# Optimization experiments

Measured on AMD Instinct MI355X. Metric: run time of the kernel, lower is better.

## Reference

```python
import jax, jax.numpy as jnp
import numpy as np

B, L, DIM, H = 2, 2048, 2048, 16
DH = DIM // H  # 128, size_per_head


def setup_inputs() -> dict:
    key = jax.random.key(0)
    k1, k2, k3, k4, k5, k6 = jax.random.split(key, 6)
    s = 0.02
    return {
        "query_tensor": jax.random.normal(k1, (B, L, DIM), jnp.float32),
        "value_tensor": jax.random.normal(k2, (B, L, DIM), jnp.float32),
        "attention_mask": jax.random.randint(k3, (B, L), 0, 2).astype(jnp.float32),
        "Wq": jax.random.normal(k4, (DIM, DIM), jnp.float32) * s,
        "Wk": jax.random.normal(k5, (DIM, DIM), jnp.float32) * s,
        "Wv": jax.random.normal(k6, (DIM, DIM), jnp.float32) * s,
    }


def reference(query_tensor, value_tensor, attention_mask, Wq, Wk, Wv):
    b, lq, dim = query_tensor.shape
    lv = value_tensor.shape[1]
    # torch Linear: x @ W.T (no bias)
    q = query_tensor @ Wq.T   # [B, Lq, DIM]
    k = value_tensor @ Wk.T   # [B, Lv, DIM]
    v = value_tensor @ Wv.T   # [B, Lv, DIM]
    # split heads -> [B, H, L, DH]
    q = q.reshape(b, lq, H, DH).transpose(0, 2, 1, 3)
    k = k.reshape(b, lv, H, DH).transpose(0, 2, 1, 3)
    v = v.reshape(b, lv, H, DH).transpose(0, 2, 1, 3)
    scores = jnp.einsum('bhqd,bhkd->bhqk', q, k) / jnp.sqrt(jnp.float32(DH))
    # multiplicative per-query mask, broadcast [B,1,Lq,1] -> [B,H,Lq,Lv]
    scores = scores * attention_mask[:, None, :, None]
    probs = jax.nn.softmax(scores, axis=-1)
    attn = jnp.einsum('bhqk,bhkd->bhqd', probs, v)  # [B,H,Lq,DH]
    return attn.transpose(0, 2, 1, 3).reshape(b, lq, dim)
```

## Files before the change

kernel.cpp:

```cpp
#include <hip/hip_runtime.h>
#include <hip/hip_bf16.h>
#include <stdint.h>

#define DIM_ 2048
#define L_   2048
#define B_   2
#define H_   16
#define DH_  128
#define NT_  32

#define QSCALE_ 0.12751743f

typedef __attribute__((ext_vector_type(4))) float fp32x4;
typedef __attribute__((ext_vector_type(8))) short s16x8;

__device__ __forceinline__ unsigned short bf16_rne(float f) {
    unsigned u = __builtin_bit_cast(unsigned, f);
    u += 0x7fffu + ((u >> 16) & 1u);
    return (unsigned short)(u >> 16);
}

__device__ __forceinline__ fp32x4 MFMA(s16x8 a, s16x8 b, fp32x4 c) {
    return __builtin_amdgcn_mfma_f32_16x16x32_bf16(a, b, c, 0, 0, 0);
}

__device__ __forceinline__ void gld16(const void* g, void* l) {
    auto gp = reinterpret_cast<const uint32_t __attribute__((address_space(1)))*>(
        reinterpret_cast<uintptr_t>(g));
    auto lp = reinterpret_cast<uint32_t __attribute__((address_space(3)))*>(
        reinterpret_cast<uintptr_t>(l));
    __builtin_amdgcn_global_load_lds(gp, lp, 16, 0, 0);
}

__device__ __forceinline__ float exp2_raw(float x) {
    float r; asm("v_exp_f32 %0, %1" : "=v"(r) : "v"(x)); return r;
}

__device__ __forceinline__ unsigned cvtpk_bf16(float a, float b) {
    unsigned r; asm("v_cvt_pk_bf16_f32 %0, %1, %2" : "=v"(r) : "v"(a), "v"(b)); return r;
}

__global__ void __launch_bounds__(256)
cvt_all(const float* __restrict__ query, const float* __restrict__ value,
        const float* __restrict__ Wq, const float* __restrict__ Wk,
        const float* __restrict__ Wv,
        unsigned short* __restrict__ qb, unsigned short* __restrict__ vb,
        unsigned short* __restrict__ wqb, unsigned short* __restrict__ wkb,
        unsigned short* __restrict__ wvb)
{
    const int total4 = 7340032;
    int i = blockIdx.x * 256 + threadIdx.x;
    const int stride = gridDim.x * 256;
    for (; i < total4; i += stride) {
        const float4* s; ushort4* d; int off; float sc = 1.0f;
        if (i < 2097152)      { s = (const float4*)query; d = (ushort4*)qb;  off = i; }
        else if (i < 4194304) { s = (const float4*)value; d = (ushort4*)vb;  off = i - 2097152; }
        else if (i < 5242880) { s = (const float4*)Wq;    d = (ushort4*)wqb; off = i - 4194304; sc = QSCALE_; }
        else if (i < 6291456) { s = (const float4*)Wk;    d = (ushort4*)wkb; off = i - 5242880; }
        else                  { s = (const float4*)Wv;    d = (ushort4*)wvb; off = i - 6291456; }
        float4 v = s[off];
        ushort4 o;
        o.x = bf16_rne(v.x * sc); o.y = bf16_rne(v.y * sc);
        o.z = bf16_rne(v.z * sc); o.w = bf16_rne(v.w * sc);
        d[off] = o;
    }
}

__global__ void __launch_bounds__(512, 2)
gemm_qkv8(const unsigned short* __restrict__ qb, const unsigned short* __restrict__ vb,
          const unsigned short* __restrict__ wqb, const unsigned short* __restrict__ wkb,
          const unsigned short* __restrict__ wvb, const float* __restrict__ mask,
          unsigned short* __restrict__ q_ws, unsigned short* __restrict__ k_ws,
          unsigned short* __restrict__ v_ws)
{
    __shared__ __align__(16) char As_[3][32768];
    __shared__ __align__(16) char Bs_[3][16384];

    const int tid  = threadIdx.x;
    const int lane = tid & 63;
    const int wid  = tid >> 6;
    const int wm   = wid >> 1;
    const int wn   = wid & 1;
    const int lr   = lane & 15;
    const int lg   = lane >> 4;

    const int g     = (blockIdx.x & 7) * 96 + (blockIdx.x >> 3);
    const int which = g >> 8;
    const int rb    = g & 255;
    const int bm    = (rb >> 4) << 8;
    const int bn    = (rb & 15) << 7;

    const unsigned short* Xb = (which == 0) ? qb : vb;
    const unsigned short* Wb = (which == 0) ? wqb : (which == 1) ? wkb : wvb;

    const int srow = tid >> 3;
    const int scol = ((tid & 7) ^ ((tid >> 3) & 7)) * 8;
    const unsigned short* gA = Xb + (size_t)(bm + srow) * DIM_ + scol;
    const unsigned short* gB = Wb + (size_t)(bn + srow) * DIM_ + scol;
    const int ldst = wid * 1024;

    const int r7   = (lr & 7) << 4;
    const int arow = (wm * 64 + lr) * 128;
    const int brow = (wn * 64 + lr) * 128;
    const int off0 = (lg << 4) ^ r7;
    const int off1 = (64 | (lg << 4)) ^ r7;

    fp32x4 acc[4][4] = {};

#define STG6(SA, SB, T) do {                                                      \
    gld16(gA + (size_t)(T) * 64,                 (SA) + ldst);                    \
    gld16(gA + (size_t)64  * DIM_ + (T) * 64,    (SA) + 8192  + ldst);            \
    gld16(gA + (size_t)128 * DIM_ + (T) * 64,    (SA) + 16384 + ldst);            \
    gld16(gA + (size_t)192 * DIM_ + (T) * 64,    (SA) + 24576 + ldst);            \
    gld16(gB + (size_t)(T) * 64,                 (SB) + ldst);                    \
    gld16(gB + (size_t)64  * DIM_ + (T) * 64,    (SB) + 8192  + ldst);            \
} while (0)

    STG6(&As_[0][0], &Bs_[0][0], 0);
    STG6(&As_[1][0], &Bs_[1][0], 1);
    asm volatile("s_waitcnt vmcnt(6)" ::: "memory");
    __builtin_amdgcn_s_barrier();

    for (int t = 0; t < NT_; ++t) {
        char* Ab = &As_[t % 3][0];
        char* Bb = &Bs_[t % 3][0];
        if (t < NT_ - 2) {
            char* An = &As_[(t + 2) % 3][0];
            char* Bn = &Bs_[(t + 2) % 3][0];
            STG6(An, Bn, t + 2);
        }

        s16x8 fa0[4], fa1[4], fb0[4], fb1[4];
        #pragma unroll
        for (int mi = 0; mi < 4; ++mi) {
            fa0[mi] = *reinterpret_cast<const s16x8*>(&Ab[arow + mi * 2048 + off0]);
            fa1[mi] = *reinterpret_cast<const s16x8*>(&Ab[arow + mi * 2048 + off1]);
        }
        #pragma unroll
        for (int nf = 0; nf < 4; ++nf) {
            fb0[nf] = *reinterpret_cast<const s16x8*>(&Bb[brow + nf * 2048 + off0]);
            fb1[nf] = *reinterpret_cast<const s16x8*>(&Bb[brow + nf * 2048 + off1]);
        }

        __builtin_amdgcn_s_setprio(1);
        #pragma unroll
        for (int mi = 0; mi < 4; ++mi)
            #pragma unroll
            for (int nf = 0; nf < 4; ++nf)
                acc[mi][nf] = MFMA(fa0[mi], fb0[nf], acc[mi][nf]);
        #pragma unroll
        for (int mi = 0; mi < 4; ++mi)
            #pragma unroll
            for (int nf = 0; nf < 4; ++nf)
                acc[mi][nf] = MFMA(fa1[mi], fb1[nf], acc[mi][nf]);
        __builtin_amdgcn_s_setprio(0);

        if (t < NT_ - 2) {
            asm volatile("s_waitcnt vmcnt(6)" ::: "memory");
            __builtin_amdgcn_s_barrier();
        } else if (t == NT_ - 2) {
            asm volatile("s_waitcnt vmcnt(0)" ::: "memory");
            __builtin_amdgcn_s_barrier();
        }
    }

    const int bb = bm >> 11;
    const size_t bh0 = (size_t)(bb * H_) * (L_ * DH_);
    const int rbase = bm + wm * 64;
    const int cbase = bn + wn * 64;

    if (which == 2) {
        #pragma unroll
        for (int mf = 0; mf < 4; ++mf) {
            int l0 = (rbase + mf * 16 + lg * 4) & (L_ - 1);
            #pragma unroll
            for (int nf = 0; nf < 4; ++nf) {
                int dc = cbase + nf * 16 + lr;
                int h = dc >> 7, d = dc & 127;
                size_t off = bh0 + (size_t)h * (L_ * DH_)
                    + (size_t)(((l0 >> 5) * 8 + (d >> 4)) * 512
                    + ((d & 15) + (((l0 >> 3) & 3) << 4)) * 8 + (l0 & 7));
                ushort4 pk;
                pk.x = bf16_rne(acc[mf][nf][0]);
                pk.y = bf16_rne(acc[mf][nf][1]);
                pk.z = bf16_rne(acc[mf][nf][2]);
                pk.w = bf16_rne(acc[mf][nf][3]);
                *reinterpret_cast<ushort4*>(&v_ws[off]) = pk;
            }
        }
    } else if (which == 1) {
        #pragma unroll
        for (int mf = 0; mf < 4; ++mf)
            #pragma unroll
            for (int rr = 0; rr < 4; ++rr) {
                int l = (rbase + mf * 16 + lg * 4 + rr) & (L_ - 1);
                #pragma unroll
                for (int nf = 0; nf < 4; ++nf) {
                    int dc = cbase + nf * 16 + lr;
                    int h = dc >> 7, d = dc & 127;
                    size_t off = bh0 + (size_t)h * (L_ * DH_)
                        + (size_t)(((l >> 4) * 4 + (d >> 5)) * 512
                        + ((l & 15) + (((d >> 3) & 3) << 4)) * 8 + (d & 7));
                    k_ws[off] = bf16_rne(acc[mf][nf][rr]);
                }
            }
    } else {
        const float* mrow = mask + bb * L_;
        #pragma unroll
        for (int mf = 0; mf < 4; ++mf)
            #pragma unroll
            for (int rr = 0; rr < 4; ++rr) {
                int l = (rbase + mf * 16 + lg * 4 + rr) & (L_ - 1);
                float mvv = mrow[l];
                #pragma unroll
                for (int nf = 0; nf < 4; ++nf) {
                    int dc = cbase + nf * 16 + lr;
                    int h = dc >> 7, d = dc & 127;
                    q_ws[bh0 + (size_t)h * (L_ * DH_) + (size_t)l * DH_ + d]
                        = bf16_rne(acc[mf][nf][rr] * mvv);
                }
            }
    }
#undef STG6
}

__global__ void __launch_bounds__(256, 2)
attn_fused3(const unsigned short* __restrict__ qw, const unsigned short* __restrict__ kfr,
            const unsigned short* __restrict__ vfr, float* __restrict__ out)
{
    __shared__ __align__(16) char Ks[2][16384];
    __shared__ __align__(16) char Pl[4][4608];

    const int tid  = threadIdx.x;
    const int lane = tid & 63;
    const int wid  = tid >> 6;
    const int lr   = lane & 15;
    const int lg   = lane >> 4;

    const int p  = (blockIdx.x & 7) * 64 + (blockIdx.x >> 3);
    const int bh = p >> 4;
    const int qt = p & 15;
    const int b  = bh >> 4;
    const int h  = bh & 15;
    const int q0 = qt * 128 + wid * 32;

    const unsigned short* qbase = qw  + (size_t)bh * (L_ * DH_);
    const unsigned short* kbase = kfr + (size_t)bh * (L_ * DH_);
    const unsigned short* vbase = vfr + (size_t)bh * (L_ * DH_);

    s16x8 qf[2][4];
    #pragma unroll
    for (int qs = 0; qs < 2; ++qs)
        #pragma unroll
        for (int kc = 0; kc < 4; ++kc)
            qf[qs][kc] = *reinterpret_cast<const s16x8*>(
                &qbase[(size_t)(q0 + qs * 16 + lr) * DH_ + kc * 32 + lg * 8]);

    s16x8 ones;
    #pragma unroll
    for (int i = 0; i < 8; ++i) ones[i] = (short)0x3F80;

    fp32x4 acc[2][8] = {};
    fp32x4 racc[2] = {};

    char* P = &Pl[wid][0];

    auto STAGE = [&](int buf, int t) {
        const unsigned short* g = kbase + (size_t)t * 8192;
        #pragma unroll
        for (int c = 0; c < 4; ++c)
            gld16(g + c * 2048 + tid * 8, &Ks[buf][c * 4096 + wid * 1024]);
    };

    STAGE(0, 0);
    __syncthreads();

    for (int t = 0; t < L_ / 64; ++t) {
        const int buf = t & 1;
        if (t + 1 < L_ / 64) STAGE(buf ^ 1, t + 1);

        s16x8 vv0[8], vv1[8];
        #pragma unroll
        for (int ds = 0; ds < 8; ++ds)
            vv0[ds] = *reinterpret_cast<const s16x8*>(
                &vbase[(size_t)t * 8192 + (0 * 8 + ds) * 512 + lane * 8]);

        fp32x4 s2[2][4] = {};
        __builtin_amdgcn_s_setprio(1);
        #pragma unroll
        for (int kvs = 0; kvs < 4; ++kvs)
            #pragma unroll
            for (int kc = 0; kc < 4; ++kc) {
                s16x8 kf = *reinterpret_cast<const s16x8*>(
                    Ks[buf] + (kvs * 4 + kc) * 1024 + lane * 16);
                s2[0][kvs] = MFMA(kf, qf[0][kc], s2[0][kvs]);
                s2[1][kvs] = MFMA(kf, qf[1][kc], s2[1][kvs]);
            }
        __builtin_amdgcn_s_setprio(0);

        #pragma unroll
        for (int qs = 0; qs < 2; ++qs)
            #pragma unroll
            for (int kvs = 0; kvs < 4; ++kvs) {
                float e0 = exp2_raw(s2[qs][kvs][0]);
                float e1 = exp2_raw(s2[qs][kvs][1]);
                float e2 = exp2_raw(s2[qs][kvs][2]);
                float e3 = exp2_raw(s2[qs][kvs][3]);
                uint2 pk;
                pk.x = cvtpk_bf16(e0, e1);
                pk.y = cvtpk_bf16(e2, e3);
                *reinterpret_cast<uint2*>(P + qs * 2304 + lr * 144 + kvs * 32 + lg * 8) = pk;
            }

        #pragma unroll
        for (int ds = 0; ds < 8; ++ds)
            vv1[ds] = *reinterpret_cast<const s16x8*>(
                &vbase[(size_t)t * 8192 + (1 * 8 + ds) * 512 + lane * 8]);

        __builtin_amdgcn_s_setprio(1);
        #pragma unroll
        for (int qs = 0; qs < 2; ++qs) {
            s16x8 pa0 = *reinterpret_cast<const s16x8*>(P + qs * 2304 + lr * 144 + 0 * 64 + lg * 16);
            s16x8 pa1 = *reinterpret_cast<const s16x8*>(P + qs * 2304 + lr * 144 + 1 * 64 + lg * 16);
            racc[qs] = MFMA(pa0, ones, racc[qs]);
            racc[qs] = MFMA(pa1, ones, racc[qs]);
            #pragma unroll
            for (int ds = 0; ds < 8; ++ds) {
                acc[qs][ds] = MFMA(pa0, vv0[ds], acc[qs][ds]);
                acc[qs][ds] = MFMA(pa1, vv1[ds], acc[qs][ds]);
            }
        }
        __builtin_amdgcn_s_setprio(0);

        __syncthreads();
    }

    #pragma unroll
    for (int qs = 0; qs < 2; ++qs) {
        float inv[4];
        #pragma unroll
        for (int r = 0; r < 4; ++r) inv[r] = 1.0f / racc[qs][r];
        #pragma unroll
        for (int ds = 0; ds < 8; ++ds)
            #pragma unroll
            for (int r = 0; r < 4; ++r)
                out[((size_t)(b * L_ + q0 + qs * 16 + lg * 4 + r)) * DIM_ + h * DH_ + ds * 16 + lr]
                    = acc[qs][ds][r] * inv[r];
    }
}

extern "C" void kernel_launch(void* const* d_in, const int* in_sizes, int n_in,
                              void* d_out, int out_size, void* d_ws, size_t ws_size,
                              hipStream_t stream) {
    const float* query = (const float*)d_in[0];
    const float* value = (const float*)d_in[1];
    const float* mask  = (const float*)d_in[2];
    const float* Wq    = (const float*)d_in[3];
    const float* Wk    = (const float*)d_in[4];
    const float* Wv    = (const float*)d_in[5];
    float* out = (float*)d_out;

    const size_t elems  = (size_t)B_ * H_ * L_ * DH_;
    const size_t welems = elems / 2;
    unsigned short* q_ws = (unsigned short*)d_ws;
    unsigned short* k_ws = q_ws + elems;
    unsigned short* v_ws = k_ws + elems;

    unsigned short* qbf  = v_ws + elems;
    unsigned short* vbf  = qbf + elems;
    unsigned short* wqbf = vbf + elems;
    unsigned short* wkbf = wqbf + welems;
    unsigned short* wvbf = wkbf + welems;

    dim3 blk(256, 1, 1);

    cvt_all<<<dim3(2048, 1, 1), blk, 0, stream>>>(query, value, Wq, Wk, Wv,
                                                  qbf, vbf, wqbf, wkbf, wvbf);
    gemm_qkv8<<<dim3(768, 1, 1), dim3(512, 1, 1), 0, stream>>>(
        qbf, vbf, wqbf, wkbf, wvbf, mask, q_ws, k_ws, v_ws);

    attn_fused3<<<dim3(512, 1, 1), blk, 0, stream>>>(q_ws, k_ws, v_ws, out);
}
```

Baseline: 203.3 us.

## Split QKV GEMM into Q GEMM and fused K/V GEMM sharing value tiles

Replaces the single 768-block QKV projection kernel with two launches. One is a 256-block Q projection. The other is a 256-block K/V kernel in which each block loads a value tile once and multiplies it against both Wk and Wv tiles, keeping two accumulator sets. This halves the global/LDS traffic for the value activations. In exchange the K/V kernel doubles its accumulator registers and drops from triple to double buffering with full vmcnt(0) waits. That may limit occupancy and latency hiding, and the extra launch serializes the Q and K/V work.

New measurement: 194.1 us, median of 3. 1.05x faster.

```diff
diff --git a/kernel.cpp b/kernel.cpp
--- a/kernel.cpp
+++ b/kernel.cpp
@@ -67,11 +67,8 @@
 }
 
 __global__ void __launch_bounds__(512, 2)
-gemm_qkv8(const unsigned short* __restrict__ qb, const unsigned short* __restrict__ vb,
-          const unsigned short* __restrict__ wqb, const unsigned short* __restrict__ wkb,
-          const unsigned short* __restrict__ wvb, const float* __restrict__ mask,
-          unsigned short* __restrict__ q_ws, unsigned short* __restrict__ k_ws,
-          unsigned short* __restrict__ v_ws)
+qgemm(const unsigned short* __restrict__ qb, const unsigned short* __restrict__ wqb,
+      const float* __restrict__ mask, unsigned short* __restrict__ q_ws)
 {
     __shared__ __align__(16) char As_[3][32768];
     __shared__ __align__(16) char Bs_[3][16384];
@@ -84,19 +81,14 @@
     const int lr   = lane & 15;
     const int lg   = lane >> 4;
 
-    const int g     = (blockIdx.x & 7) * 96 + (blockIdx.x >> 3);
-    const int which = g >> 8;
-    const int rb    = g & 255;
-    const int bm    = (rb >> 4) << 8;
-    const int bn    = (rb & 15) << 7;
-
-    const unsigned short* Xb = (which == 0) ? qb : vb;
-    const unsigned short* Wb = (which == 0) ? wqb : (which == 1) ? wkb : wvb;
+    const int rb = (blockIdx.x & 7) * 32 + (blockIdx.x >> 3);
+    const int bm = (rb >> 4) << 8;
+    const int bn = (rb & 15) << 7;
 
     const int srow = tid >> 3;
     const int scol = ((tid & 7) ^ ((tid >> 3) & 7)) * 8;
-    const unsigned short* gA = Xb + (size_t)(bm + srow) * DIM_ + scol;
-    const unsigned short* gB = Wb + (size_t)(bn + srow) * DIM_ + scol;
+    const unsigned short* gA = qb  + (size_t)(bm + srow) * DIM_ + scol;
+    const unsigned short* gB = wqb + (size_t)(bn + srow) * DIM_ + scol;
     const int ldst = wid * 1024;
 
     const int r7   = (lr & 7) << 4;
@@ -125,9 +117,7 @@
         char* Ab = &As_[t % 3][0];
         char* Bb = &Bs_[t % 3][0];
         if (t < NT_ - 2) {
-            char* An = &As_[(t + 2) % 3][0];
-            char* Bn = &Bs_[(t + 2) % 3][0];
-            STG6(An, Bn, t + 2);
+            STG6(&As_[(t + 2) % 3][0], &Bs_[(t + 2) % 3][0], t + 2);
         }
 
         s16x8 fa0[4], fa1[4], fb0[4], fb1[4];
@@ -163,65 +153,166 @@
             __builtin_amdgcn_s_barrier();
         }
     }
+#undef STG6
 
     const int bb = bm >> 11;
     const size_t bh0 = (size_t)(bb * H_) * (L_ * DH_);
     const int rbase = bm + wm * 64;
     const int cbase = bn + wn * 64;
-
-    if (which == 2) {
-        #pragma unroll
-        for (int mf = 0; mf < 4; ++mf) {
-            int l0 = (rbase + mf * 16 + lg * 4) & (L_ - 1);
+    const float* mrow = mask + bb * L_;
+
+    #pragma unroll
+    for (int mf = 0; mf < 4; ++mf)
+        #pragma unroll
+        for (int rr = 0; rr < 4; ++rr) {
+            int l = (rbase + mf * 16 + lg * 4 + rr) & (L_ - 1);
+            float mvv = mrow[l];
+            #pragma unroll
+            for (int nf = 0; nf < 4; ++nf) {
+                int dc = cbase + nf * 16 + lr;
+                int h = dc >> 7, d = dc & 127;
+                q_ws[bh0 + (size_t)h * (L_ * DH_) + (size_t)l * DH_ + d]
+                    = bf16_rne(acc[mf][nf][rr] * mvv);
+            }
+        }
+}
+
+__global__ void __launch_bounds__(512, 2)
+kvgemm(const unsigned short* __restrict__ vb, const unsigned short* __restrict__ wkb,
+       const unsigned short* __restrict__ wvb,
+       unsigned short* __restrict__ k_ws, unsigned short* __restrict__ v_ws)
+{
+    __shared__ __align__(16) char As_[2][32768];
+    __shared__ __align__(16) char Bks_[2][16384];
+    __shared__ __align__(16) char Bvs_[2][16384];
+
+    const int tid  = threadIdx.x;
+    const int lane = tid & 63;
+    const int wid  = tid >> 6;
+    const int wm   = wid >> 1;
+    const int wn   = wid & 1;
+    const int lr   = lane & 15;
+    const int lg   = lane >> 4;
+
+    const int rb = (blockIdx.x & 7) * 32 + (blockIdx.x >> 3);
+    const int bm = (rb >> 4) << 8;
+    const int bn = (rb & 15) << 7;
+
+    const int srow = tid >> 3;
+    const int scol = ((tid & 7) ^ ((tid >> 3) & 7)) * 8;
+    const unsigned short* gA  = vb  + (size_t)(bm + srow) * DIM_ + scol;
+    const unsigned short* gBk = wkb + (size_t)(bn + srow) * DIM_ + scol;
+    const unsigned short* gBv = wvb + (size_t)(bn + srow) * DIM_ + scol;
+    const int ldst = wid * 1024;
+
+    const int r7   = (lr & 7) << 4;
+    const int arow = (wm * 64 + lr) * 128;
+    const int brow = (wn * 64 + lr) * 128;
+    const int off0 = (lg << 4) ^ r7;
+    const int off1 = (64 | (lg << 4)) ^ r7;
+
+    fp32x4 acck[4][4] = {};
+    fp32x4 accv[4][4] = {};
+
+#define STG8(BUF, T) do {                                                         \
+    gld16(gA  + (size_t)(T) * 64,               &As_[BUF][ldst]);                 \
+    gld16(gA  + (size_t)64  * DIM_ + (T) * 64,  &As_[BUF][8192  + ldst]);         \
+    gld16(gA  + (size_t)128 * DIM_ + (T) * 64,  &As_[BUF][16384 + ldst]);         \
+    gld16(gA  + (size_t)192 * DIM_ + (T) * 64,  &As_[BUF][24576 + ldst]);         \
+    gld16(gBk + (size_t)(T) * 64,               &Bks_[BUF][ldst]);                \
+    gld16(gBk + (size_t)64  * DIM_ + (T) * 64,  &Bks_[BUF][8192 + ldst]);         \
+    gld16(gBv + (size_t)(T) * 64,               &Bvs_[BUF][ldst]);                \
+    gld16(gBv + (size_t)64  * DIM_ + (T) * 64,  &Bvs_[BUF][8192 + ldst]);         \
+} while (0)
+
+    STG8(0, 0);
+    asm volatile("s_waitcnt vmcnt(0)" ::: "memory");
+    __builtin_amdgcn_s_barrier();
+
+    for (int t = 0; t < NT_; ++t) {
+        const int buf = t & 1;
+        if (t + 1 < NT_) STG8(buf ^ 1, t + 1);
+
+        char* Ab  = &As_[buf][0];
+        char* Bkb = &Bks_[buf][0];
+        char* Bvb = &Bvs_[buf][0];
+
+        #pragma unroll
+        for (int kk = 0; kk < 2; ++kk) {
+            const int o = kk ? off1 : off0;
+            s16x8 fa[4], fk[4];
+            #pragma unroll
+            for (int mi = 0; mi < 4; ++mi)
+                fa[mi] = *reinterpret_cast<const s16x8*>(&Ab[arow + mi * 2048 + o]);
+            #pragma unroll
+            for (int nf = 0; nf < 4; ++nf)
+                fk[nf] = *reinterpret_cast<const s16x8*>(&Bkb[brow + nf * 2048 + o]);
+            __builtin_amdgcn_s_setprio(1);
+            #pragma unroll
+            for (int mi = 0; mi < 4; ++mi)
+                #pragma unroll
+                for (int nf = 0; nf < 4; ++nf)
+                    acck[mi][nf] = MFMA(fa[mi], fk[nf], acck[mi][nf]);
+            __builtin_amdgcn_s_setprio(0);
+            s16x8 fv[4];
+            #pragma unroll
+            for (int nf = 0; nf < 4; ++nf)
+                fv[nf] = *reinterpret_cast<const s16x8*>(&Bvb[brow + nf * 2048 + o]);
+            __builtin_amdgcn_s_setprio(1);
+            #pragma unroll
+            for (int mi = 0; mi < 4; ++mi)
+                #pragma unroll
+                for (int nf = 0; nf < 4; ++nf)
+                    accv[mi][nf] = MFMA(fa[mi], fv[nf], accv[mi][nf]);
+            __builtin_amdgcn_s_setprio(0);
+        }
+
+        if (t + 1 < NT_) {
+            asm volatile("s_waitcnt vmcnt(0)" ::: "memory");
+            __builtin_amdgcn_s_barrier();
+        }
+    }
+#undef STG8
+
+    const int bb = bm >> 11;
+    const size_t bh0 = (size_t)(bb * H_) * (L_ * DH_);
+    const int rbase = bm + wm * 64;
+    const int cbase = bn + wn * 64;
+
+    #pragma unroll
+    for (int mf = 0; mf < 4; ++mf)
+        #pragma unroll
+        for (int rr = 0; rr < 4; ++rr) {
+            int l = (rbase + mf * 16 + lg * 4 + rr) & (L_ - 1);
             #pragma unroll
             for (int nf = 0; nf < 4; ++nf) {
                 int dc = cbase + nf * 16 + lr;
                 int h = dc >> 7, d = dc & 127;
                 size_t off = bh0 + (size_t)h * (L_ * DH_)
-                    + (size_t)(((l0 >> 5) * 8 + (d >> 4)) * 512
-                    + ((d & 15) + (((l0 >> 3) & 3) << 4)) * 8 + (l0 & 7));
-                ushort4 pk;
-                pk.x = bf16_rne(acc[mf][nf][0]);
-                pk.y = bf16_rne(acc[mf][nf][1]);
-                pk.z = bf16_rne(acc[mf][nf][2]);
-                pk.w = bf16_rne(acc[mf][nf][3]);
-                *reinterpret_cast<ushort4*>(&v_ws[off]) = pk;
+                    + (size_t)(((l >> 4) * 4 + (d >> 5)) * 512
+                    + ((l & 15) + (((d >> 3) & 3) << 4)) * 8 + (d & 7));
+                k_ws[off] = bf16_rne(acck[mf][nf][rr]);
             }
         }
-    } else if (which == 1) {
-        #pragma unroll
-        for (int mf = 0; mf < 4; ++mf)
-            #pragma unroll
-            for (int rr = 0; rr < 4; ++rr) {
-                int l = (rbase + mf * 16 + lg * 4 + rr) & (L_ - 1);
-                #pragma unroll
-                for (int nf = 0; nf < 4; ++nf) {
-                    int dc = cbase + nf * 16 + lr;
-                    int h = dc >> 7, d = dc & 127;
-                    size_t off = bh0 + (size_t)h * (L_ * DH_)
-                        + (size_t)(((l >> 4) * 4 + (d >> 5)) * 512
-                        + ((l & 15) + (((d >> 3) & 3) << 4)) * 8 + (d & 7));
-                    k_ws[off] = bf16_rne(acc[mf][nf][rr]);
-                }
-            }
-    } else {
-        const float* mrow = mask + bb * L_;
-        #pragma unroll
-        for (int mf = 0; mf < 4; ++mf)
-            #pragma unroll
-            for (int rr = 0; rr < 4; ++rr) {
-                int l = (rbase + mf * 16 + lg * 4 + rr) & (L_ - 1);
-                float mvv = mrow[l];
-                #pragma unroll
-                for (int nf = 0; nf < 4; ++nf) {
-                    int dc = cbase + nf * 16 + lr;
-                    int h = dc >> 7, d = dc & 127;
-                    q_ws[bh0 + (size_t)h * (L_ * DH_) + (size_t)l * DH_ + d]
-                        = bf16_rne(acc[mf][nf][rr] * mvv);
-                }
-            }
-    }
-#undef STG6
+
+    #pragma unroll
+    for (int mf = 0; mf < 4; ++mf) {
+        int l0 = (rbase + mf * 16 + lg * 4) & (L_ - 1);
+        #pragma unroll
+        for (int nf = 0; nf < 4; ++nf) {
+            int dc = cbase + nf * 16 + lr;
+            int h = dc >> 7, d = dc & 127;
+            size_t off = bh0 + (size_t)h * (L_ * DH_)
+                + (size_t)(((l0 >> 5) * 8 + (d >> 4)) * 512
+                + ((d & 15) + (((l0 >> 3) & 3) << 4)) * 8 + (l0 & 7));
+            ushort4 pk;
+            pk.x = bf16_rne(accv[mf][nf][0]);
+            pk.y = bf16_rne(accv[mf][nf][1]);
+            pk.z = bf16_rne(accv[mf][nf][2]);
+            pk.w = bf16_rne(accv[mf][nf][3]);
+            *reinterpret_cast<ushort4*>(&v_ws[off]) = pk;
+        }
+    }
 }
 
 __global__ void __launch_bounds__(256, 2)
@@ -376,8 +467,8 @@
 
     cvt_all<<<dim3(2048, 1, 1), blk, 0, stream>>>(query, value, Wq, Wk, Wv,
                                                   qbf, vbf, wqbf, wkbf, wvbf);
-    gemm_qkv8<<<dim3(768, 1, 1), dim3(512, 1, 1), 0, stream>>>(
-        qbf, vbf, wqbf, wkbf, wvbf, mask, q_ws, k_ws, v_ws);
+    qgemm<<<dim3(256, 1, 1), dim3(512, 1, 1), 0, stream>>>(qbf, wqbf, mask, q_ws);
+    kvgemm<<<dim3(256, 1, 1), dim3(512, 1, 1), 0, stream>>>(vbf, wkbf, wvbf, k_ws, v_ws);
 
     attn_fused3<<<dim3(512, 1, 1), blk, 0, stream>>>(q_ws, k_ws, v_ws, out);
 }
```
